# Kernel optimization log

Measured on AMD Instinct MI355X. Metric: run time of the kernel, lower is better.

The kernel has to match this reference:

```python
import jax, jax.numpy as jnp
import numpy as np

N_NODES = 50000
N_EDGES = 1600000
IN_CH = 256
LAT = 32
HID = 64
OUT_CH = 256
GAT_H = 32  # GAT hidden dims [32, 32], heads=1


def setup_inputs() -> dict:
    key = jax.random.key(0)
    ks = jax.random.split(key, 30)
    nrm = lambda k, shape, s=0.05: jax.random.normal(k, shape, dtype=jnp.float32) * s
    inp = {}
    inp["x"] = jax.random.normal(ks[0], (N_NODES, IN_CH), dtype=jnp.float32)
    inp["edge_index"] = jax.random.randint(ks[1], (2, N_EDGES), 0, N_NODES)
    # GAT layer 1: IN_CH -> 32 (heads=1), layer 2: 32 -> 32, final linear 32 -> LAT
    inp["W_g1"] = nrm(ks[2], (IN_CH, GAT_H)); inp["as_g1"] = nrm(ks[3], (GAT_H,)); inp["ad_g1"] = nrm(ks[4], (GAT_H,)); inp["b_g1"] = jnp.zeros((GAT_H,), jnp.float32)
    inp["W_g2"] = nrm(ks[5], (GAT_H, GAT_H)); inp["as_g2"] = nrm(ks[6], (GAT_H,)); inp["ad_g2"] = nrm(ks[7], (GAT_H,)); inp["b_g2"] = jnp.zeros((GAT_H,), jnp.float32)
    inp["W_gf"] = nrm(ks[8], (GAT_H, LAT)); inp["b_gf"] = jnp.zeros((LAT,), jnp.float32)
    inp["W_m1"] = nrm(ks[9], (IN_CH, HID)); inp["b_m1"] = jnp.zeros((HID,), jnp.float32); inp["g_m1"] = jnp.ones((HID,), jnp.float32); inp["be_m1"] = jnp.zeros((HID,), jnp.float32)
    inp["W_m2"] = nrm(ks[10], (HID, HID)); inp["b_m2"] = jnp.zeros((HID,), jnp.float32); inp["g_m2"] = jnp.ones((HID,), jnp.float32); inp["be_m2"] = jnp.zeros((HID,), jnp.float32)
    inp["W_m3"] = nrm(ks[11], (HID, LAT)); inp["b_m3"] = jnp.zeros((LAT,), jnp.float32); inp["g_m3"] = jnp.ones((LAT,), jnp.float32); inp["be_m3"] = jnp.zeros((LAT,), jnp.float32)
    # final linear LAT -> OUT_CH + ReLU
    inp["W_f"] = nrm(ks[12], (LAT, OUT_CH)); inp["b_f"] = jnp.zeros((OUT_CH,), jnp.float32)
    return inp


def _bn_relu(h, g, b):
    # BatchNorm1d in training mode: batch stats, biased variance, eps=1e-5
    m = jnp.mean(h, axis=0)
    v = jnp.var(h, axis=0)
    return jax.nn.relu((h - m) * jax.lax.rsqrt(v + 1e-5) * g + b)


def _gat(h_in, src, dst, W, a_s, a_d, b):
    # PyG GATConv (heads=1): edge (src j -> dst i), e = LeakyReLU(a_src.Wx_j + a_dst.Wx_i)
    N = h_in.shape[0]
    h = h_in @ W                                   # [N, F]
    e = jax.nn.leaky_relu((h @ a_s)[src] + (h @ a_d)[dst], 0.2)  # [E]
    m = jax.ops.segment_max(e, dst, num_segments=N)              # scatter-softmax over incoming edges
    ex = jnp.exp(e - m[dst])
    den = jax.ops.segment_sum(ex, dst, num_segments=N)
    alpha = ex / den[dst]
    out = jax.ops.segment_sum(alpha[:, None] * h[src], dst, num_segments=N)
    return out + b


def reference(x, edge_index, W_g1, as_g1, ad_g1, b_g1, W_g2, as_g2, ad_g2, b_g2, W_gf, b_gf, W_m1, b_m1, g_m1, be_m1, W_m2, b_m2, g_m2, be_m2, W_m3, b_m3, g_m3, be_m3, W_f, b_f):
    N = x.shape[0]
    loops = jnp.arange(N)
    src = jnp.concatenate([edge_index[0], loops])  # PyG add_self_loops=True
    dst = jnp.concatenate([edge_index[1], loops])
    r = _bn_relu(x @ W_m1 + b_m1, g_m1, be_m1)
    r = _bn_relu(r @ W_m2 + b_m2, g_m2, be_m2)
    r = _bn_relu(r @ W_m3 + b_m3, g_m3, be_m3)
    # GAT interpolation branch (dropout inactive in eval)
    h = jax.nn.relu(_gat(x, src, dst, W_g1, as_g1, ad_g1, b_g1))
    h = jax.nn.relu(_gat(h, src, dst, W_g2, as_g2, ad_g2, b_g2))
    h = h @ W_gf + b_gf
    # blend with alphas = 0.5 constant vector
    out = 0.5 * r + 0.5 * h
    return jax.nn.relu(out @ W_f + b_f)
```

## Files before the change

### kernel.cpp

```cpp
#include <hip/hip_runtime.h>

#define NNODES 50000
#define NEDGES 1600000
#define NBUCK 196
#define BIN_CH 4096
#define CNT_CH 4096

typedef __attribute__((ext_vector_type(4))) float f32x4;
typedef __attribute__((ext_vector_type(8))) short short8;

__device__ __forceinline__ float leaky02(float x) { return x > 0.f ? x : 0.2f * x; }

__device__ __forceinline__ int block_incl_scan(int v, int* sh) {
  int t = threadIdx.x;
  sh[t] = v;
  __syncthreads();
  for (int d = 1; d < 256; d <<= 1) {
    int u = (t >= d) ? sh[t - d] : 0;
    __syncthreads();
    sh[t] += u;
    __syncthreads();
  }
  return sh[t];
}

__global__ __launch_bounds__(256) void k_b0(const int* __restrict__ dst,
                                            int* __restrict__ gcnt, int E) {
  __shared__ int hist[256];
  int t = threadIdx.x;
  hist[t] = 0;
  __syncthreads();
  int base0 = blockIdx.x * CNT_CH;
#pragma unroll
  for (int r = 0; r < CNT_CH / 256; ++r) {
    int idx = base0 + r * 256 + t;
    if (idx < E) atomicAdd(&hist[dst[idx] >> 8], 1);
  }
  __syncthreads();
  if (t < NBUCK && hist[t]) atomicAdd(&gcnt[t], hist[t]);
}

__global__ __launch_bounds__(256) void k_b1(const int* __restrict__ gcnt,
                                            int* __restrict__ base,
                                            int* __restrict__ cursor) {
  __shared__ int sh[256];
  int t = threadIdx.x;
  int v = (t < NBUCK) ? gcnt[t] : 0;
  int incl = block_incl_scan(v, sh);
  if (t < NBUCK) {
    base[t] = incl - v;
    cursor[t] = incl - v;
  }
  if (t == 255) base[NBUCK] = NEDGES;
}

__global__ __launch_bounds__(256) void k_bin(const int* __restrict__ src,
                                             const int* __restrict__ dst,
                                             int* __restrict__ cursor,
                                             unsigned* __restrict__ binned, int E) {
  __shared__ int hist[256];
  __shared__ int cur[256];
  int t = threadIdx.x;
  int base0 = blockIdx.x * BIN_CH;
  unsigned pk[BIN_CH / 256];
  hist[t] = 0;
  __syncthreads();
#pragma unroll
  for (int r = 0; r < BIN_CH / 256; ++r) {
    int idx = base0 + r * 256 + t;
    if (idx < E) {
      unsigned p = ((unsigned)dst[idx] << 16) | (unsigned)src[idx];
      pk[r] = p;
      atomicAdd(&hist[p >> 24], 1);
    }
  }
  __syncthreads();
  if (t < NBUCK && hist[t]) cur[t] = atomicAdd(&cursor[t], hist[t]);
  __syncthreads();
#pragma unroll
  for (int r = 0; r < BIN_CH / 256; ++r) {
    int idx = base0 + r * 256 + t;
    if (idx < E) {
      unsigned p = pk[r];
      int pos = atomicAdd(&cur[p >> 24], 1);
      binned[pos] = p;
    }
  }
}

__global__ __launch_bounds__(256) void k_sort(const unsigned* __restrict__ binned,
                                              const int* __restrict__ base,
                                              int* __restrict__ deg,
                                              int* __restrict__ offs,
                                              int* __restrict__ csr) {
  __shared__ int hist[256];
  __shared__ int scanbuf[256];
  __shared__ int cur[256];
  int t = threadIdx.x;
  int b = blockIdx.x;
  int lo = base[b], hi = base[b + 1];
  int node0 = b << 8;
  hist[t] = 0;
  __syncthreads();
  for (int i = lo + t; i < hi; i += 256)
    atomicAdd(&hist[(binned[i] >> 16) & 255], 1);
  __syncthreads();
  int h = hist[t];
  int incl = block_incl_scan(h, scanbuf);
  int excl = incl - h;
  int node = node0 + t;
  if (node < NNODES) {
    deg[node] = h;
    offs[node] = lo + excl;
  }
  cur[t] = lo + excl;
  __syncthreads();
  for (int i = lo + t; i < hi; i += 256) {
    unsigned p = binned[i];
    int pos = atomicAdd(&cur[(p >> 16) & 255], 1);
    csr[pos] = (int)(p & 0xFFFFu);
  }
}

template <int K, int NC, int TN, int SPLIT, bool BN, bool STATS, int ROWS>
__global__ __launch_bounds__(256) void k_gemm(
    const float* __restrict__ A, const float* __restrict__ bn_sum,
    const float* __restrict__ bn_sq, const float* __restrict__ bn_gamma,
    const float* __restrict__ bn_beta, float invM,
    const float* __restrict__ B0, const float* __restrict__ B1,
    const float* __restrict__ bias0,
    float* __restrict__ out0, float* __restrict__ out1,
    float* __restrict__ gsum, float* __restrict__ gsq, int M) {
  constexpr int KC = 64;
  constexpr int RPT = ROWS / 16;
  __shared__ float As[ROWS * KC];
  __shared__ float Bs[KC * NC];
  __shared__ float scS[BN ? K : 4];
  __shared__ float shS[BN ? K : 4];
  const int tid = threadIdx.x;
  const int row0 = blockIdx.x * ROWS;
  const int cg = tid & 15;
  const int rowg = (tid >> 4) & 15;
  const int swz = (rowg & 3) << 2;

  if constexpr (BN) {
    if (tid < K) {
      float mean = bn_sum[tid] * invM;
      float var = bn_sq[tid] * invM - mean * mean;
      float rs = rsqrtf(var + 1e-5f);
      float sc = rs * bn_gamma[tid];
      scS[tid] = sc;
      shS[tid] = bn_beta[tid] - mean * sc;
    }
    __syncthreads();
  }

  float acc[RPT][TN];
#pragma unroll
  for (int r = 0; r < RPT; ++r)
#pragma unroll
    for (int j = 0; j < TN; ++j) acc[r][j] = 0.f;

  constexpr int KB = KC / 4;
  for (int k0 = 0; k0 < K; k0 += KC) {
#pragma unroll
    for (int it = 0; it < (ROWS * KB) / 256; ++it) {
      int idx = tid + it * 256;
      int row = idx / KB;
      int kb = idx % KB;
      float4 v = make_float4(0.f, 0.f, 0.f, 0.f);
      int grow = row0 + row;
      if (grow < M) {
        v = *reinterpret_cast<const float4*>(&A[(size_t)grow * K + k0 + kb * 4]);
        if constexpr (BN) {
          int kb4 = k0 + kb * 4;
          float4 sc = *reinterpret_cast<const float4*>(&scS[kb4]);
          float4 sf = *reinterpret_cast<const float4*>(&shS[kb4]);
          v.x = fmaxf(v.x * sc.x + sf.x, 0.f);
          v.y = fmaxf(v.y * sc.y + sf.y, 0.f);
          v.z = fmaxf(v.z * sc.z + sf.z, 0.f);
          v.w = fmaxf(v.w * sc.w + sf.w, 0.f);
        }
      }
      *reinterpret_cast<float4*>(&As[row * KC + ((kb ^ (row & 3)) * 4)]) = v;
    }
    {
      constexpr int KB0 = SPLIT / 4;
#pragma unroll
      for (int it = 0; it < (KC * KB0) / 256; ++it) {
        int idx = tid + it * 256;
        int kk = idx / KB0;
        int cb = idx % KB0;
        float4 v = *reinterpret_cast<const float4*>(&B0[(size_t)(k0 + kk) * SPLIT + cb * 4]);
        *reinterpret_cast<float4*>(&Bs[kk * NC + cb * 4]) = v;
      }
    }
    if constexpr (NC > SPLIT) {
      constexpr int W1 = NC - SPLIT;
      constexpr int KB1 = W1 / 4;
#pragma unroll
      for (int it = 0; it < (KC * KB1) / 256; ++it) {
        int idx = tid + it * 256;
        int kk = idx / KB1;
        int cb = idx % KB1;
        float4 v = *reinterpret_cast<const float4*>(&B1[(size_t)(k0 + kk) * W1 + cb * 4]);
        *reinterpret_cast<float4*>(&Bs[kk * NC + SPLIT + cb * 4]) = v;
      }
    }
    __syncthreads();
    for (int kk = 0; kk < KC; kk += 4) {
      float4 a[RPT];
#pragma unroll
      for (int r = 0; r < RPT; ++r)
        a[r] = *reinterpret_cast<const float4*>(&As[(rowg + 16 * r) * KC + (kk ^ swz)]);
      float b[4][TN];
#pragma unroll
      for (int i = 0; i < 4; ++i)
#pragma unroll
        for (int j = 0; j < TN; ++j) b[i][j] = Bs[(kk + i) * NC + cg * TN + j];
#pragma unroll
      for (int r = 0; r < RPT; ++r)
#pragma unroll
        for (int j = 0; j < TN; ++j) {
          acc[r][j] += a[r].x * b[0][j];
          acc[r][j] += a[r].y * b[1][j];
          acc[r][j] += a[r].z * b[2][j];
          acc[r][j] += a[r].w * b[3][j];
        }
    }
    __syncthreads();
  }
  float bias_r[TN];
#pragma unroll
  for (int j = 0; j < TN; ++j) {
    int c = cg * TN + j;
    bias_r[j] = (c < SPLIT) ? bias0[c] : 0.f;
  }
  float cs[TN], cq[TN];
#pragma unroll
  for (int j = 0; j < TN; ++j) { cs[j] = 0.f; cq[j] = 0.f; }
#pragma unroll
  for (int r = 0; r < RPT; ++r) {
    int grow = row0 + rowg + 16 * r;
    if (grow < M) {
#pragma unroll
      for (int j = 0; j < TN; ++j) {
        int c = cg * TN + j;
        if (c < SPLIT) {
          float v = acc[r][j] + bias_r[j];
          out0[(size_t)grow * SPLIT + c] = v;
          if (STATS) { cs[j] += v; cq[j] += v * v; }
        } else {
          out1[(size_t)grow * (NC - SPLIT) + (c - SPLIT)] = acc[r][j];
        }
      }
    }
  }
  if constexpr (STATS) {
#pragma unroll
    for (int j = 0; j < TN; ++j) {
      cs[j] += __shfl_xor(cs[j], 16);
      cs[j] += __shfl_xor(cs[j], 32);
      cq[j] += __shfl_xor(cq[j], 16);
      cq[j] += __shfl_xor(cq[j], 32);
    }
    float* red = Bs;
    int wave = tid >> 6;
    int lane = tid & 63;
    if (lane < 16) {
#pragma unroll
      for (int j = 0; j < TN; ++j) {
        int c = cg * TN + j;
        if (c < SPLIT) {
          red[wave * 2 * SPLIT + c] = cs[j];
          red[wave * 2 * SPLIT + SPLIT + c] = cq[j];
        }
      }
    }
    __syncthreads();
    if (tid < SPLIT) {
      float s = red[tid] + red[2 * SPLIT + tid] + red[4 * SPLIT + tid] + red[6 * SPLIT + tid];
      atomicAdd(&gsum[tid], s);
    } else if (tid < 2 * SPLIT) {
      int c = tid - SPLIT;
      float q = red[SPLIT + c] + red[3 * SPLIT + c] + red[5 * SPLIT + c] + red[7 * SPLIT + c];
      atomicAdd(&gsq[c], q);
    }
  }
}

__global__ __launch_bounds__(512) void k_bsplit(const float* __restrict__ Wm,
                                                const float* __restrict__ Wg,
                                                unsigned short* __restrict__ Bt) {
  int b = blockIdx.x;
  int c = b / 6, cf = b % 6;
  int t = threadIdx.x;
  int lane = t >> 3, j = t & 7;
  int lg = lane >> 4, lc = lane & 15;
  int k = c * 32 + lg * 8 + j;
  int col = cf * 16 + lc;
  float v = (col < 64) ? Wm[k * 64 + col] : Wg[k * 32 + (col - 64)];
  unsigned bb = __float_as_uint(v);
  unsigned h = bb & 0xffff0000u;
  float lo = v - __uint_as_float(h);
  Bt[(size_t)(b * 2 + 0) * 512 + t] = (unsigned short)(h >> 16);
  Bt[(size_t)(b * 2 + 1) * 512 + t] = (unsigned short)(__float_as_uint(lo) >> 16);
}

union U16 { uint4 u; short8 s; };
__device__ __forceinline__ short8 as_s8(uint4 u) { U16 t; t.u = u; return t.s; }

__device__ __forceinline__ void split2(float x0, float x1, unsigned& h, unsigned& l) {
  unsigned b0 = __float_as_uint(x0), b1 = __float_as_uint(x1);
  unsigned h0 = b0 & 0xffff0000u, h1 = b1 & 0xffff0000u;
  h = (h0 >> 16) | h1;
  float l0 = x0 - __uint_as_float(h0);
  float l1 = x1 - __uint_as_float(h1);
  l = (__float_as_uint(l0) >> 16) | (__float_as_uint(l1) & 0xffff0000u);
}

__device__ __forceinline__ void split8(const float4& a, const float4& b,
                                       short8& hi, short8& lo) {
  uint4 h, l;
  split2(a.x, a.y, h.x, l.x);
  split2(a.z, a.w, h.y, l.y);
  split2(b.x, b.y, h.z, l.z);
  split2(b.z, b.w, h.w, l.w);
  hi = as_s8(h);
  lo = as_s8(l);
}

__device__ __forceinline__ void gload16(const float* g, float* l) {
  __builtin_amdgcn_global_load_lds(
      (const __attribute__((address_space(1))) void*)g,
      (__attribute__((address_space(3))) void*)l, 16, 0, 0);
}

__global__ __launch_bounds__(128) void k_gemm1_mfma(
    const float* __restrict__ A, const unsigned short* __restrict__ Bt,
    const float* __restrict__ bias0,
    float* __restrict__ out0, float* __restrict__ out1,
    float* __restrict__ gsum, float* __restrict__ gsq, int M) {
  __shared__ float As[2][64 * 32];
  __shared__ float red[256];
  const int tid = threadIdx.x;
  const int wv = tid >> 6;
  const int lane = tid & 63;
  const int lg = lane >> 4;
  const int lc = lane & 15;
  const int rowb = blockIdx.x * 64;

  const int srow = lane >> 3;
  const int sslot = (lane & 7) ^ srow;

  const int rl0 = wv * 32 + lc;
  const int rl1 = rl0 + 16;
  const int p00 = (lg * 2) ^ (rl0 & 7), p01 = (lg * 2 + 1) ^ (rl0 & 7);
  const int p10 = (lg * 2) ^ (rl1 & 7), p11 = (lg * 2 + 1) ^ (rl1 & 7);

  f32x4 acc[2][6];
#pragma unroll
  for (int rf = 0; rf < 2; ++rf)
#pragma unroll
    for (int cf = 0; cf < 6; ++cf) acc[rf][cf] = (f32x4){0.f, 0.f, 0.f, 0.f};

#pragma unroll
  for (int it = 0; it < 4; ++it) {
    const int si = wv * 4 + it;
    int grow = rowb + si * 8 + srow;
    grow = grow < M ? grow : M - 1;
    gload16(A + (size_t)grow * 256 + sslot * 4, &As[0][si * 256]);
  }
  __syncthreads();

#pragma unroll
  for (int c = 0; c < 8; ++c) {
    const int buf = c & 1;
    if (c < 7) {
#pragma unroll
      for (int it = 0; it < 4; ++it) {
        const int si = wv * 4 + it;
        int grow = rowb + si * 8 + srow;
        grow = grow < M ? grow : M - 1;
        gload16(A + (size_t)grow * 256 + (c + 1) * 32 + sslot * 4,
                &As[buf ^ 1][si * 256]);
      }
    }
    uint4 bhr[6], blr[6];
    const unsigned short* bp = Bt + (size_t)c * 6144 + lane * 8;
#pragma unroll
    for (int cf = 0; cf < 6; ++cf) {
      bhr[cf] = *reinterpret_cast<const uint4*>(bp + cf * 1024);
      blr[cf] = *reinterpret_cast<const uint4*>(bp + cf * 1024 + 512);
    }
    float4 a00 = *reinterpret_cast<const float4*>(&As[buf][rl0 * 32 + p00 * 4]);
    float4 a01 = *reinterpret_cast<const float4*>(&As[buf][rl0 * 32 + p01 * 4]);
    float4 a10 = *reinterpret_cast<const float4*>(&As[buf][rl1 * 32 + p10 * 4]);
    float4 a11 = *reinterpret_cast<const float4*>(&As[buf][rl1 * 32 + p11 * 4]);
    short8 ah[2], al[2];
    split8(a00, a01, ah[0], al[0]);
    split8(a10, a11, ah[1], al[1]);
#pragma unroll
    for (int rf = 0; rf < 2; ++rf)
#pragma unroll
      for (int cf = 0; cf < 6; ++cf) {
        short8 bh = as_s8(bhr[cf]), bl = as_s8(blr[cf]);
        acc[rf][cf] = __builtin_amdgcn_mfma_f32_16x16x32_bf16(ah[rf], bh, acc[rf][cf], 0, 0, 0);
        acc[rf][cf] = __builtin_amdgcn_mfma_f32_16x16x32_bf16(al[rf], bh, acc[rf][cf], 0, 0, 0);
        acc[rf][cf] = __builtin_amdgcn_mfma_f32_16x16x32_bf16(ah[rf], bl, acc[rf][cf], 0, 0, 0);
      }
    __syncthreads();
  }

  float bias_r[4];
#pragma unroll
  for (int cf = 0; cf < 4; ++cf) bias_r[cf] = bias0[cf * 16 + lc];
  float cs[4] = {0.f, 0.f, 0.f, 0.f}, cq[4] = {0.f, 0.f, 0.f, 0.f};
#pragma unroll
  for (int rf = 0; rf < 2; ++rf) {
    int rbase = rowb + wv * 32 + rf * 16 + lg * 4;
#pragma unroll
    for (int i = 0; i < 4; ++i) {
      int row = rbase + i;
      if (row < M) {
#pragma unroll
        for (int cf = 0; cf < 4; ++cf) {
          float v = acc[rf][cf][i] + bias_r[cf];
          out0[(size_t)row * 64 + cf * 16 + lc] = v;
          cs[cf] += v;
          cq[cf] += v * v;
        }
#pragma unroll
        for (int cf = 4; cf < 6; ++cf)
          out1[(size_t)row * 32 + (cf - 4) * 16 + lc] = acc[rf][cf][i];
      }
    }
  }
#pragma unroll
  for (int cf = 0; cf < 4; ++cf) {
    cs[cf] += __shfl_xor(cs[cf], 16);
    cs[cf] += __shfl_xor(cs[cf], 32);
    cq[cf] += __shfl_xor(cq[cf], 16);
    cq[cf] += __shfl_xor(cq[cf], 32);
  }
  if (lg == 0) {
#pragma unroll
    for (int cf = 0; cf < 4; ++cf) {
      red[wv * 128 + cf * 16 + lc] = cs[cf];
      red[wv * 128 + 64 + cf * 16 + lc] = cq[cf];
    }
  }
  __syncthreads();
  if (tid < 64) {
    atomicAdd(&gsum[tid], red[tid] + red[128 + tid]);
  } else {
    int cc = tid - 64;
    atomicAdd(&gsq[cc], red[64 + cc] + red[192 + cc]);
  }
}

__global__ __launch_bounds__(256) void k_sdot(const float* __restrict__ g,
                                              const float* __restrict__ as_,
                                              const float* __restrict__ ad_,
                                              float* __restrict__ sv,
                                              float* __restrict__ dv, int N) {
  int lane = threadIdx.x & 31;
  int row = blockIdx.x * 8 + (threadIdx.x >> 5);
  if (row >= N) return;
  float v = g[(size_t)row * 32 + lane];
  float a = v * as_[lane];
  float b = v * ad_[lane];
#pragma unroll
  for (int w = 16; w >= 1; w >>= 1) {
    a += __shfl_xor(a, w);
    b += __shfl_xor(b, w);
  }
  if (lane == 0) {
    sv[row] = a;
    dv[row] = b;
  }
}

__global__ __launch_bounds__(256) void k_gat_agg(
    const float* __restrict__ h, const float* __restrict__ sv,
    const float* __restrict__ dv, const int* __restrict__ offs,
    const int* __restrict__ deg, const int* __restrict__ csr,
    const float* __restrict__ bias, float* __restrict__ out, int N) {
  int lane = threadIdx.x & 31;
  int node = blockIdx.x * 8 + (threadIdx.x >> 5);
  if (node >= N) return;
  int start = offs[node];
  int cnt = deg[node];
  float di = dv[node];
  float ex0 = __expf(leaky02(sv[node] + di));
  float den = ex0;
  float acc = ex0 * h[(size_t)node * 32 + lane];
  int k = 0;
  for (; k + 8 <= cnt; k += 8) {
    int j0 = csr[start + k + 0], j1 = csr[start + k + 1];
    int j2 = csr[start + k + 2], j3 = csr[start + k + 3];
    int j4 = csr[start + k + 4], j5 = csr[start + k + 5];
    int j6 = csr[start + k + 6], j7 = csr[start + k + 7];
    float s0 = sv[j0], s1 = sv[j1], s2 = sv[j2], s3 = sv[j3];
    float s4 = sv[j4], s5 = sv[j5], s6 = sv[j6], s7 = sv[j7];
    float h0 = h[(size_t)j0 * 32 + lane], h1 = h[(size_t)j1 * 32 + lane];
    float h2 = h[(size_t)j2 * 32 + lane], h3 = h[(size_t)j3 * 32 + lane];
    float h4 = h[(size_t)j4 * 32 + lane], h5 = h[(size_t)j5 * 32 + lane];
    float h6 = h[(size_t)j6 * 32 + lane], h7 = h[(size_t)j7 * 32 + lane];
    float e0 = __expf(leaky02(s0 + di)), e1 = __expf(leaky02(s1 + di));
    float e2 = __expf(leaky02(s2 + di)), e3 = __expf(leaky02(s3 + di));
    float e4 = __expf(leaky02(s4 + di)), e5 = __expf(leaky02(s5 + di));
    float e6 = __expf(leaky02(s6 + di)), e7 = __expf(leaky02(s7 + di));
    den += ((e0 + e1) + (e2 + e3)) + ((e4 + e5) + (e6 + e7));
    acc += e0 * h0 + e1 * h1 + e2 * h2 + e3 * h3;
    acc += e4 * h4 + e5 * h5 + e6 * h6 + e7 * h7;
  }
  for (; k < cnt; ++k) {
    int j = csr[start + k];
    float ex = __expf(leaky02(sv[j] + di));
    den += ex;
    acc += ex * h[(size_t)j * 32 + lane];
  }
  out[(size_t)node * 32 + lane] = fmaxf(acc / den + bias[lane], 0.f);
}

__global__ __launch_bounds__(256) void k_small_gemm_sd(
    const float* __restrict__ hin, const float* __restrict__ W,
    const float* __restrict__ as_, const float* __restrict__ ad_,
    float* __restrict__ gout, float* __restrict__ sv, float* __restrict__ dv,
    int N) {
  __shared__ float Ws[32][32];
  {
    int t = threadIdx.x;
#pragma unroll
    for (int r = 0; r < 4; ++r) {
      int idx = t + r * 256;
      Ws[idx >> 5][idx & 31] = W[idx];
    }
  }
  __syncthreads();
  int lane = threadIdx.x & 31;
  int row = blockIdx.x * 8 + (threadIdx.x >> 5);
  if (row >= N) return;
  float hv = hin[(size_t)row * 32 + lane];
  float acc = 0.f;
#pragma unroll
  for (int k = 0; k < 32; ++k) acc += __shfl(hv, k, 32) * Ws[k][lane];
  gout[(size_t)row * 32 + lane] = acc;
  float a = acc * as_[lane];
  float b = acc * ad_[lane];
#pragma unroll
  for (int w = 16; w >= 1; w >>= 1) {
    a += __shfl_xor(a, w);
    b += __shfl_xor(b, w);
  }
  if (lane == 0) {
    sv[row] = a;
    dv[row] = b;
  }
}

__global__ __launch_bounds__(256) void k_final2(
    const float* __restrict__ mlp3, const float* __restrict__ sum3,
    const float* __restrict__ sq3, const float* __restrict__ g3,
    const float* __restrict__ be3, float invM, const float* __restrict__ h2,
    const float* __restrict__ Wgf, const float* __restrict__ bgf,
    const float* __restrict__ Wf, const float* __restrict__ bf,
    float* __restrict__ out, int N) {
  __shared__ float WfS[32 * 256];
  __shared__ float Bl[64][36];
  __shared__ float WgfS[32][33];
  __shared__ float colS[3][32];
  const int t = threadIdx.x;
  const int row0 = blockIdx.x * 64;

  {
    const float4* src = reinterpret_cast<const float4*>(Wf);
    float4* dst = reinterpret_cast<float4*>(WfS);
#pragma unroll
    for (int r = 0; r < 8; ++r) dst[t + r * 256] = src[t + r * 256];
  }
#pragma unroll
  for (int r = 0; r < 4; ++r) {
    int idx = t + r * 256;
    WgfS[idx >> 5][idx & 31] = Wgf[idx];
  }
  if (t < 32) {
    float mean = sum3[t] * invM;
    float var = sq3[t] * invM - mean * mean;
    float rs = rsqrtf(var + 1e-5f);
    float sc = rs * g3[t];
    colS[0][t] = sc;
    colS[1][t] = be3[t] - mean * sc;
    colS[2][t] = bgf[t];
  }
#pragma unroll
  for (int r = 0; r < 2; ++r) {
    int idx = t + r * 256;
    int row = idx >> 3;
    int k4 = idx & 7;
    int grow = row0 + row;
    float4 v = make_float4(0.f, 0.f, 0.f, 0.f);
    if (grow < N) v = *reinterpret_cast<const float4*>(&h2[(size_t)grow * 32 + k4 * 4]);
    *reinterpret_cast<float4*>(&Bl[row][k4 * 4]) = v;
  }
  __syncthreads();

  const int col = t & 31;
  const int rb = t >> 5;
  float w[32];
#pragma unroll
  for (int k = 0; k < 32; ++k) w[k] = WgfS[k][col];
  float bl[8];
#pragma unroll
  for (int r = 0; r < 8; ++r) {
    int row = rb + 8 * r;
    float a = colS[2][col];
#pragma unroll
    for (int k4 = 0; k4 < 8; ++k4) {
      float4 hv = *reinterpret_cast<const float4*>(&Bl[row][k4 * 4]);
      a += hv.x * w[k4 * 4 + 0] + hv.y * w[k4 * 4 + 1] +
           hv.z * w[k4 * 4 + 2] + hv.w * w[k4 * 4 + 3];
    }
    int grow = row0 + row;
    float pre = (grow < N) ? mlp3[(size_t)grow * 32 + col] : 0.f;
    float rv = fmaxf(pre * colS[0][col] + colS[1][col], 0.f);
    bl[r] = 0.5f * rv + 0.5f * a;
  }
  __syncthreads();
#pragma unroll
  for (int r = 0; r < 8; ++r) Bl[rb + 8 * r][col] = bl[r];
  __syncthreads();

  const int cg = t & 31;
  const int rowg = t >> 5;
  const float4* Wf4 = reinterpret_cast<const float4*>(WfS);
  float4 acc0[8], acc1[8];
#pragma unroll
  for (int r = 0; r < 8; ++r) {
    acc0[r] = make_float4(0.f, 0.f, 0.f, 0.f);
    acc1[r] = make_float4(0.f, 0.f, 0.f, 0.f);
  }
  for (int k = 0; k < 32; k += 4) {
    float4 a[8];
#pragma unroll
    for (int r = 0; r < 8; ++r)
      a[r] = *reinterpret_cast<const float4*>(&Bl[rowg + 8 * r][k]);
    float4 b0[4], b1[4];
#pragma unroll
    for (int i = 0; i < 4; ++i) {
      b0[i] = Wf4[(k + i) * 64 + cg];
      b1[i] = Wf4[(k + i) * 64 + cg + 32];
    }
#pragma unroll
    for (int r = 0; r < 8; ++r) {
      float av[4] = {a[r].x, a[r].y, a[r].z, a[r].w};
#pragma unroll
      for (int i = 0; i < 4; ++i) {
        acc0[r].x += av[i] * b0[i].x;
        acc0[r].y += av[i] * b0[i].y;
        acc0[r].z += av[i] * b0[i].z;
        acc0[r].w += av[i] * b0[i].w;
        acc1[r].x += av[i] * b1[i].x;
        acc1[r].y += av[i] * b1[i].y;
        acc1[r].z += av[i] * b1[i].z;
        acc1[r].w += av[i] * b1[i].w;
      }
    }
  }
  float4 bfA = reinterpret_cast<const float4*>(bf)[cg];
  float4 bfB = reinterpret_cast<const float4*>(bf)[cg + 32];
  float4* out4 = reinterpret_cast<float4*>(out);
#pragma unroll
  for (int r = 0; r < 8; ++r) {
    int grow = row0 + rowg + 8 * r;
    if (grow < N) {
      float4 o0 = acc0[r], o1 = acc1[r];
      o0.x = fmaxf(o0.x + bfA.x, 0.f); o0.y = fmaxf(o0.y + bfA.y, 0.f);
      o0.z = fmaxf(o0.z + bfA.z, 0.f); o0.w = fmaxf(o0.w + bfA.w, 0.f);
      o1.x = fmaxf(o1.x + bfB.x, 0.f); o1.y = fmaxf(o1.y + bfB.y, 0.f);
      o1.z = fmaxf(o1.z + bfB.z, 0.f); o1.w = fmaxf(o1.w + bfB.w, 0.f);
      out4[(size_t)grow * 64 + cg] = o0;
      out4[(size_t)grow * 64 + cg + 32] = o1;
    }
  }
}

extern "C" void kernel_launch(void* const* d_in, const int* in_sizes, int n_in,
                              void* d_out, int out_size, void* d_ws, size_t ws_size,
                              hipStream_t stream) {
  const float* x = (const float*)d_in[0];
  const int* edge = (const int*)d_in[1];
  const float* W_g1 = (const float*)d_in[2];
  const float* as_g1 = (const float*)d_in[3];
  const float* ad_g1 = (const float*)d_in[4];
  const float* b_g1 = (const float*)d_in[5];
  const float* W_g2 = (const float*)d_in[6];
  const float* as_g2 = (const float*)d_in[7];
  const float* ad_g2 = (const float*)d_in[8];
  const float* b_g2 = (const float*)d_in[9];
  const float* W_gf = (const float*)d_in[10];
  const float* b_gf = (const float*)d_in[11];
  const float* W_m1 = (const float*)d_in[12];
  const float* b_m1 = (const float*)d_in[13];
  const float* g_m1 = (const float*)d_in[14];
  const float* be_m1 = (const float*)d_in[15];
  const float* W_m2 = (const float*)d_in[16];
  const float* b_m2 = (const float*)d_in[17];
  const float* g_m2 = (const float*)d_in[18];
  const float* be_m2 = (const float*)d_in[19];
  const float* W_m3 = (const float*)d_in[20];
  const float* b_m3 = (const float*)d_in[21];
  const float* g_m3 = (const float*)d_in[22];
  const float* be_m3 = (const float*)d_in[23];
  const float* W_f = (const float*)d_in[24];
  const float* b_f = (const float*)d_in[25];
  float* out = (float*)d_out;

  const int N = NNODES, E = NEDGES;
  const float invM = 1.f / N;
  const int* esrc = edge;
  const int* edst = edge + E;

  float* ws = (float*)d_ws;
  float* g1 = ws;
  float* mlp1 = g1 + (size_t)N * 32;
  float* mlp2 = mlp1 + (size_t)N * 64;
  float* mlp3 = mlp2 + (size_t)N * 64;
  float* h1 = mlp3 + (size_t)N * 32;
  float* g2 = h1 + (size_t)N * 32;
  float* h2 = g2 + (size_t)N * 32;
  float* s1 = h2 + (size_t)N * 32;
  float* d1 = s1 + N;
  float* s2 = d1 + N;
  float* d2 = s2 + N;
  float* stats = d2 + N;
  float* sum1 = stats, *sq1 = stats + 64;
  float* sum2 = stats + 128, *sq2 = stats + 192;
  float* sum3 = stats + 256, *sq3 = stats + 288;
  int* ip = (int*)(stats + 384);
  int* gcnt = ip;
  int* base = gcnt + 256;
  int* cursor = base + 256;
  int* deg = cursor + 256;
  int* offs = deg + N;
  int* csr = offs + N;
  unsigned* binned = (unsigned*)mlp2;
  unsigned short* Bt = (unsigned short*)((char*)mlp2 + (size_t)E * 4);

  hipMemsetAsync(gcnt, 0, 256 * sizeof(int), stream);
  hipMemsetAsync(stats, 0, 384 * sizeof(float), stream);

  k_bsplit<<<48, 512, 0, stream>>>(W_m1, W_g1, Bt);

  k_b0<<<(E + CNT_CH - 1) / CNT_CH, 256, 0, stream>>>(edst, gcnt, E);
  k_b1<<<1, 256, 0, stream>>>(gcnt, base, cursor);
  k_bin<<<(E + BIN_CH - 1) / BIN_CH, 256, 0, stream>>>(esrc, edst, cursor, binned, E);
  k_sort<<<NBUCK, 256, 0, stream>>>(binned, base, deg, offs, csr);

  const int GB64 = (N + 63) / 64;
  const int GB128 = (N + 127) / 128;

  k_gemm1_mfma<<<GB64, 128, 0, stream>>>(x, Bt, b_m1, mlp1, g1, sum1, sq1, N);
  k_sdot<<<(N + 7) / 8, 256, 0, stream>>>(g1, as_g1, ad_g1, s1, d1, N);
  k_gat_agg<<<(N + 7) / 8, 256, 0, stream>>>(g1, s1, d1, offs, deg, csr, b_g1, h1, N);

  k_gemm<64, 64, 4, 64, true, true, 128><<<GB128, 256, 0, stream>>>(
      mlp1, sum1, sq1, g_m1, be_m1, invM, W_m2, nullptr, b_m2,
      mlp2, nullptr, sum2, sq2, N);

  k_small_gemm_sd<<<(N + 7) / 8, 256, 0, stream>>>(h1, W_g2, as_g2, ad_g2, g2, s2, d2, N);
  k_gat_agg<<<(N + 7) / 8, 256, 0, stream>>>(g2, s2, d2, offs, deg, csr, b_g2, h2, N);

  k_gemm<64, 32, 2, 32, true, true, 128><<<GB128, 256, 0, stream>>>(
      mlp2, sum2, sq2, g_m2, be_m2, invM, W_m3, nullptr, b_m3,
      mlp3, nullptr, sum3, sq3, N);

  k_final2<<<(N + 63) / 64, 256, 0, stream>>>(mlp3, sum3, sq3, g_m3, be_m3, invM,
                                              h2, W_gf, b_gf, W_f, b_f, out, N);
}
```

Baseline: 398.2 us.

## Split gemm1 MFMA block across four waves with 2x2 tile and 64-wide K chunks

The first GEMM kernel (x @ [W_m1|W_g1]) now runs 256 threads per block, with waves arranged 2x2 over rows and column groups, so each wave computes 3 column fragments instead of 6. The K loop is restaged in 64-wide chunks (4 iterations instead of 8), which halves the number of barriers and doubles the LDS tile. The aim is to add waves per block for latency hiding and to shorten each wave's MFMA chain. In exchange, each row's A fragment is read from LDS by two waves, and the BN statistics reduction becomes slightly more involved.

```diff
diff --git a/kernel.cpp b/kernel.cpp
--- a/kernel.cpp
+++ b/kernel.cpp
@@ -293,11 +293,11 @@
                                                 const float* __restrict__ Wg,
                                                 unsigned short* __restrict__ Bt) {
   int b = blockIdx.x;
-  int c = b / 6, cf = b % 6;
+  int cc = b / 6, cf = b % 6;
   int t = threadIdx.x;
   int lane = t >> 3, j = t & 7;
   int lg = lane >> 4, lc = lane & 15;
-  int k = c * 32 + lg * 8 + j;
+  int k = cc * 32 + lg * 8 + j;
   int col = cf * 16 + lc;
   float v = (col < 64) ? Wm[k * 64 + col] : Wg[k * 32 + (col - 64)];
   unsigned bb = __float_as_uint(v);
@@ -336,126 +336,154 @@
       (__attribute__((address_space(3))) void*)l, 16, 0, 0);
 }
 
-__global__ __launch_bounds__(128) void k_gemm1_mfma(
+__global__ __launch_bounds__(256) void k_gemm1_mfma(
     const float* __restrict__ A, const unsigned short* __restrict__ Bt,
     const float* __restrict__ bias0,
     float* __restrict__ out0, float* __restrict__ out1,
     float* __restrict__ gsum, float* __restrict__ gsq, int M) {
-  __shared__ float As[2][64 * 32];
-  __shared__ float red[256];
+  __shared__ float As[2][64 * 64];
+  __shared__ float red[512];
   const int tid = threadIdx.x;
   const int wv = tid >> 6;
   const int lane = tid & 63;
   const int lg = lane >> 4;
   const int lc = lane & 15;
+  const int wr = wv >> 1;
+  const int wc = wv & 1;
   const int rowb = blockIdx.x * 64;
 
-  const int srow = lane >> 3;
-  const int sslot = (lane & 7) ^ srow;
-
-  const int rl0 = wv * 32 + lc;
+  const int sp = lane & 15;
+  const int sr4 = lane >> 4;
+
+  const int rl0 = wr * 32 + lc;
   const int rl1 = rl0 + 16;
-  const int p00 = (lg * 2) ^ (rl0 & 7), p01 = (lg * 2 + 1) ^ (rl0 & 7);
-  const int p10 = (lg * 2) ^ (rl1 & 7), p11 = (lg * 2 + 1) ^ (rl1 & 7);
-
-  f32x4 acc[2][6];
+
+  f32x4 acc[2][3];
 #pragma unroll
   for (int rf = 0; rf < 2; ++rf)
 #pragma unroll
-    for (int cf = 0; cf < 6; ++cf) acc[rf][cf] = (f32x4){0.f, 0.f, 0.f, 0.f};
-
-#pragma unroll
-  for (int it = 0; it < 4; ++it) {
-    const int si = wv * 4 + it;
-    int grow = rowb + si * 8 + srow;
+    for (int j = 0; j < 3; ++j) acc[rf][j] = (f32x4){0.f, 0.f, 0.f, 0.f};
+
+#pragma unroll
+  for (int q = 0; q < 4; ++q) {
+    int r = wv * 16 + q * 4 + sr4;
+    int grow = rowb + r;
     grow = grow < M ? grow : M - 1;
-    gload16(A + (size_t)grow * 256 + sslot * 4, &As[0][si * 256]);
-  }
-  __syncthreads();
-
-#pragma unroll
-  for (int c = 0; c < 8; ++c) {
+    int s = sp ^ (r & 7);
+    gload16(A + (size_t)grow * 256 + s * 4, &As[0][(wv * 16 + q * 4) * 64]);
+  }
+  __syncthreads();
+
+#pragma unroll
+  for (int c = 0; c < 4; ++c) {
     const int buf = c & 1;
-    if (c < 7) {
-#pragma unroll
-      for (int it = 0; it < 4; ++it) {
-        const int si = wv * 4 + it;
-        int grow = rowb + si * 8 + srow;
+    if (c < 3) {
+#pragma unroll
+      for (int q = 0; q < 4; ++q) {
+        int r = wv * 16 + q * 4 + sr4;
+        int grow = rowb + r;
         grow = grow < M ? grow : M - 1;
-        gload16(A + (size_t)grow * 256 + (c + 1) * 32 + sslot * 4,
-                &As[buf ^ 1][si * 256]);
-      }
-    }
-    uint4 bhr[6], blr[6];
-    const unsigned short* bp = Bt + (size_t)c * 6144 + lane * 8;
-#pragma unroll
-    for (int cf = 0; cf < 6; ++cf) {
-      bhr[cf] = *reinterpret_cast<const uint4*>(bp + cf * 1024);
-      blr[cf] = *reinterpret_cast<const uint4*>(bp + cf * 1024 + 512);
-    }
-    float4 a00 = *reinterpret_cast<const float4*>(&As[buf][rl0 * 32 + p00 * 4]);
-    float4 a01 = *reinterpret_cast<const float4*>(&As[buf][rl0 * 32 + p01 * 4]);
-    float4 a10 = *reinterpret_cast<const float4*>(&As[buf][rl1 * 32 + p10 * 4]);
-    float4 a11 = *reinterpret_cast<const float4*>(&As[buf][rl1 * 32 + p11 * 4]);
-    short8 ah[2], al[2];
-    split8(a00, a01, ah[0], al[0]);
-    split8(a10, a11, ah[1], al[1]);
-#pragma unroll
-    for (int rf = 0; rf < 2; ++rf)
-#pragma unroll
-      for (int cf = 0; cf < 6; ++cf) {
-        short8 bh = as_s8(bhr[cf]), bl = as_s8(blr[cf]);
-        acc[rf][cf] = __builtin_amdgcn_mfma_f32_16x16x32_bf16(ah[rf], bh, acc[rf][cf], 0, 0, 0);
-        acc[rf][cf] = __builtin_amdgcn_mfma_f32_16x16x32_bf16(al[rf], bh, acc[rf][cf], 0, 0, 0);
-        acc[rf][cf] = __builtin_amdgcn_mfma_f32_16x16x32_bf16(ah[rf], bl, acc[rf][cf], 0, 0, 0);
-      }
+        int s = sp ^ (r & 7);
+        gload16(A + (size_t)grow * 256 + (c + 1) * 64 + s * 4,
+                &As[buf ^ 1][(wv * 16 + q * 4) * 64]);
+      }
+    }
+    uint4 bhr[2][3], blr[2][3];
+#pragma unroll
+    for (int ks = 0; ks < 2; ++ks) {
+      int cc = c * 2 + ks;
+#pragma unroll
+      for (int j = 0; j < 3; ++j) {
+        const unsigned short* bp =
+            Bt + (size_t)((cc * 6 + wc * 3 + j) * 2) * 512 + lane * 8;
+        bhr[ks][j] = *reinterpret_cast<const uint4*>(bp);
+        blr[ks][j] = *reinterpret_cast<const uint4*>(bp + 512);
+      }
+    }
+#pragma unroll
+    for (int ks = 0; ks < 2; ++ks) {
+      const int s0 = ks * 8 + lg * 2;
+      float4 a00 = *reinterpret_cast<const float4*>(
+          &As[buf][rl0 * 64 + ((s0) ^ (rl0 & 7)) * 4]);
+      float4 a01 = *reinterpret_cast<const float4*>(
+          &As[buf][rl0 * 64 + ((s0 + 1) ^ (rl0 & 7)) * 4]);
+      float4 a10 = *reinterpret_cast<const float4*>(
+          &As[buf][rl1 * 64 + ((s0) ^ (rl1 & 7)) * 4]);
+      float4 a11 = *reinterpret_cast<const float4*>(
+          &As[buf][rl1 * 64 + ((s0 + 1) ^ (rl1 & 7)) * 4]);
+      short8 ah0, al0, ah1, al1;
+      split8(a00, a01, ah0, al0);
+      split8(a10, a11, ah1, al1);
+#pragma unroll
+      for (int j = 0; j < 3; ++j) {
+        short8 bh = as_s8(bhr[ks][j]), bl = as_s8(blr[ks][j]);
+        acc[0][j] = __builtin_amdgcn_mfma_f32_16x16x32_bf16(ah0, bh, acc[0][j], 0, 0, 0);
+        acc[0][j] = __builtin_amdgcn_mfma_f32_16x16x32_bf16(al0, bh, acc[0][j], 0, 0, 0);
+        acc[0][j] = __builtin_amdgcn_mfma_f32_16x16x32_bf16(ah0, bl, acc[0][j], 0, 0, 0);
+        acc[1][j] = __builtin_amdgcn_mfma_f32_16x16x32_bf16(ah1, bh, acc[1][j], 0, 0, 0);
+        acc[1][j] = __builtin_amdgcn_mfma_f32_16x16x32_bf16(al1, bh, acc[1][j], 0, 0, 0);
+        acc[1][j] = __builtin_amdgcn_mfma_f32_16x16x32_bf16(ah1, bl, acc[1][j], 0, 0, 0);
+      }
+    }
     __syncthreads();
   }
 
-  float bias_r[4];
-#pragma unroll
-  for (int cf = 0; cf < 4; ++cf) bias_r[cf] = bias0[cf * 16 + lc];
-  float cs[4] = {0.f, 0.f, 0.f, 0.f}, cq[4] = {0.f, 0.f, 0.f, 0.f};
+  red[tid] = 0.f;
+  red[tid + 256] = 0.f;
+  __syncthreads();
+
+  float bias_r[3];
+#pragma unroll
+  for (int j = 0; j < 3; ++j) {
+    int gcf = wc * 3 + j;
+    bias_r[j] = (gcf < 4) ? bias0[gcf * 16 + lc] : 0.f;
+  }
+  float cs[3] = {0.f, 0.f, 0.f}, cq[3] = {0.f, 0.f, 0.f};
 #pragma unroll
   for (int rf = 0; rf < 2; ++rf) {
-    int rbase = rowb + wv * 32 + rf * 16 + lg * 4;
+    int rbase = rowb + wr * 32 + rf * 16 + lg * 4;
 #pragma unroll
     for (int i = 0; i < 4; ++i) {
       int row = rbase + i;
       if (row < M) {
 #pragma unroll
-        for (int cf = 0; cf < 4; ++cf) {
-          float v = acc[rf][cf][i] + bias_r[cf];
-          out0[(size_t)row * 64 + cf * 16 + lc] = v;
-          cs[cf] += v;
-          cq[cf] += v * v;
+        for (int j = 0; j < 3; ++j) {
+          int gcf = wc * 3 + j;
+          if (gcf < 4) {
+            float v = acc[rf][j][i] + bias_r[j];
+            out0[(size_t)row * 64 + gcf * 16 + lc] = v;
+            cs[j] += v;
+            cq[j] += v * v;
+          } else {
+            out1[(size_t)row * 32 + (gcf - 4) * 16 + lc] = acc[rf][j][i];
+          }
         }
-#pragma unroll
-        for (int cf = 4; cf < 6; ++cf)
-          out1[(size_t)row * 32 + (cf - 4) * 16 + lc] = acc[rf][cf][i];
-      }
-    }
-  }
-#pragma unroll
-  for (int cf = 0; cf < 4; ++cf) {
-    cs[cf] += __shfl_xor(cs[cf], 16);
-    cs[cf] += __shfl_xor(cs[cf], 32);
-    cq[cf] += __shfl_xor(cq[cf], 16);
-    cq[cf] += __shfl_xor(cq[cf], 32);
+      }
+    }
+  }
+#pragma unroll
+  for (int j = 0; j < 3; ++j) {
+    cs[j] += __shfl_xor(cs[j], 16);
+    cs[j] += __shfl_xor(cs[j], 32);
+    cq[j] += __shfl_xor(cq[j], 16);
+    cq[j] += __shfl_xor(cq[j], 32);
   }
   if (lg == 0) {
 #pragma unroll
-    for (int cf = 0; cf < 4; ++cf) {
-      red[wv * 128 + cf * 16 + lc] = cs[cf];
-      red[wv * 128 + 64 + cf * 16 + lc] = cq[cf];
+    for (int j = 0; j < 3; ++j) {
+      int gcf = wc * 3 + j;
+      if (gcf < 4) {
+        red[wv * 128 + gcf * 16 + lc] = cs[j];
+        red[wv * 128 + 64 + gcf * 16 + lc] = cq[j];
+      }
     }
   }
   __syncthreads();
   if (tid < 64) {
-    atomicAdd(&gsum[tid], red[tid] + red[128 + tid]);
-  } else {
-    int cc = tid - 64;
-    atomicAdd(&gsq[cc], red[64 + cc] + red[192 + cc]);
+    atomicAdd(&gsum[tid], red[tid] + red[128 + tid] + red[256 + tid] + red[384 + tid]);
+  } else if (tid < 128) {
+    int cc2 = tid - 64;
+    atomicAdd(&gsq[cc2], red[64 + cc2] + red[192 + cc2] + red[320 + cc2] + red[448 + cc2]);
   }
 }
 
@@ -761,7 +789,7 @@
   const int GB64 = (N + 63) / 64;
   const int GB128 = (N + 127) / 128;
 
-  k_gemm1_mfma<<<GB64, 128, 0, stream>>>(x, Bt, b_m1, mlp1, g1, sum1, sq1, N);
+  k_gemm1_mfma<<<GB64, 256, 0, stream>>>(x, Bt, b_m1, mlp1, g1, sum1, sq1, N);
   k_sdot<<<(N + 7) / 8, 256, 0, stream>>>(g1, as_g1, ad_g1, s1, d1, N);
   k_gat_agg<<<(N + 7) / 8, 256, 0, stream>>>(g1, s1, d1, offs, deg, csr, b_g1, h1, N);
 
```

Measured after the change: 399.2 us. About the same (+0.2%).
